# Optimization experiments

Hardware: AMD Instinct MI355X
Metric: run time of the kernel (lower is better)

The kernel has to match this reference:

```python
import jax, jax.numpy as jnp
import numpy as np

# Config matching init_kwargs: layer_nb=1 -> stride 16, image 608x608 -> 38x38 grid
B, CIN, H, W = 32, 512, 38, 38
NA, NC = 3, 80
STRIDE = 16.0
ANCHORS = np.array([[30.0, 61.0], [62.0, 45.0], [59.0, 119.0]], dtype=np.float32)


def setup_inputs() -> dict:
    key = jax.random.key(0)
    k1, k2, k3 = jax.random.split(key, 3)
    xin = jax.random.normal(k1, (B, CIN, H, W), dtype=jnp.float32)
    # 1x1 conv weight stored as (out_ch, in_ch); out_ch = NA*(NC+5) = 255
    conv_w = jax.random.normal(k2, (NA * (NC + 5), CIN), dtype=jnp.float32) * 0.02
    conv_b = jax.random.normal(k3, (NA * (NC + 5),), dtype=jnp.float32) * 0.01
    return {"xin": xin, "conv_w": conv_w, "conv_b": conv_b}


def reference(xin, conv_w, conv_b):
    # 1x1 conv == channel GEMM; fuse the NCHW->NHWC permute into the einsum
    fm = jnp.einsum('bchw,oc->bhwo', xin, conv_w) + conv_b  # [B,H,W,255]
    fm = fm.reshape(B, H, W, NA, NC + 5)
    tx, ty, tw, th = fm[..., 0], fm[..., 1], fm[..., 2], fm[..., 3]
    # grid offsets (precomputed via broadcasting instead of per-call numpy rebuild)
    x_off = jnp.arange(W, dtype=fm.dtype)[None, None, :, None]   # broadcast over B,H,NA
    y_off = jnp.arange(H, dtype=fm.dtype)[None, :, None, None]   # broadcast over B,W,NA
    anchors = jnp.asarray(ANCHORS, dtype=fm.dtype)               # [NA,2]
    bx = (jax.nn.sigmoid(tx) + x_off) * STRIDE
    by = (jax.nn.sigmoid(ty) + y_off) * STRIDE
    bw = jnp.exp(tw) * anchors[:, 0]
    bh = jnp.exp(th) * anchors[:, 1]
    boxes = jnp.stack([bx, by, bw, bh], axis=-1)                 # [B,H,W,NA,4]
    # concat decoded boxes with raw objectness + class logits -> [B,H,W,NA,85]
    return jnp.concatenate([boxes, fm[..., 4:]], axis=-1)
```

## Files before the change

### kernel.cpp

```cpp
#include <hip/hip_runtime.h>
#include <cstdint>
#include <cstddef>

#define CIN_K  512
#define WW_    38
#define BHW    1444
#define NOUT   255
#define MTOT   46208

#define KCH    256
#define ROW_E  260
#define EP_DW  260

typedef __attribute__((ext_vector_type(8))) short  bf16x8;
typedef __attribute__((ext_vector_type(4))) float  floatx4;

static __device__ __forceinline__ unsigned f2bf(float f) {
    unsigned u = __builtin_bit_cast(unsigned, f);
    return (u + 0x7FFFu + ((u >> 16) & 1u)) >> 16;
}

__global__ void conv_w_to_bf16(const float* __restrict__ cw,
                               unsigned short* __restrict__ wb) {
    int tg   = blockIdx.x * 256 + threadIdx.x;
    int base = tg * 8;
    int n    = base >> 9;
    unsigned rr[4] = {0u, 0u, 0u, 0u};
    if (n < NOUT) {
        float4 v0 = *(const float4*)(cw + base);
        float4 v1 = *(const float4*)(cw + base + 4);
        rr[0] = f2bf(v0.x) | (f2bf(v0.y) << 16);
        rr[1] = f2bf(v0.z) | (f2bf(v0.w) << 16);
        rr[2] = f2bf(v1.x) | (f2bf(v1.y) << 16);
        rr[3] = f2bf(v1.z) | (f2bf(v1.w) << 16);
    }
    *(uint4*)(wb + base) = *(uint4*)rr;
}

__global__ __launch_bounds__(256, 4)
void yolo_head(const float* __restrict__ xin,
               const unsigned short* __restrict__ wb,
               const float* __restrict__ cb,
               float* __restrict__ out)
{
    __shared__ unsigned smem[64 * (ROW_E / 2)];
    unsigned short* As = (unsigned short*)smem;

    const int t    = threadIdx.x;
    const int w    = t >> 6;
    const int lane = t & 63;
    const int l15  = lane & 15;
    const int q    = lane >> 4;
    const int m0   = blockIdx.x * 64;

    const int mq4 = (t & 15) * 4;
    const int kq4 = (t >> 4) * 4;
    const int m4  = m0 + mq4;
    const int bi  = m4 / BHW;
    const int hw  = m4 - bi * BHW;
    const float* pb0 = xin + (size_t)bi * (CIN_K * BHW) + hw;

    floatx4 acc[4][4];
#pragma unroll
    for (int i = 0; i < 4; ++i)
#pragma unroll
        for (int j = 0; j < 4; ++j)
            acc[i][j] = (floatx4){0.f, 0.f, 0.f, 0.f};

    const unsigned short* pbw = wb + (size_t)(w * 64 + l15) * CIN_K + q * 8;

#pragma unroll
    for (int ck = 0; ck < 2; ++ck) {
        if (ck) __syncthreads();

#pragma unroll
        for (int it = 0; it < 4; ++it) {
            const int kl = it * 64 + kq4;
            alignas(16) float vv[4][4];
#pragma unroll
            for (int kk = 0; kk < 4; ++kk)
                *(float4*)&vv[kk][0] =
                    *(const float4*)(pb0 + (size_t)(ck * KCH + kl + kk) * BHW);
#pragma unroll
            for (int r = 0; r < 4; ++r) {
                unsigned lo = f2bf(vv[0][r]) | (f2bf(vv[1][r]) << 16);
                unsigned hi = f2bf(vv[2][r]) | (f2bf(vv[3][r]) << 16);
                uint2 pk = make_uint2(lo, hi);
                *(uint2*)(&As[(mq4 + r) * ROW_E + kl]) = pk;
            }
        }
        __syncthreads();

#pragma unroll
        for (int kc = 0; kc < 8; ++kc) {
            bf16x8 bfr[4], af[4];
#pragma unroll
            for (int j = 0; j < 4; ++j) {
                uint4 bv = *(const uint4*)(pbw + (size_t)j * 16 * CIN_K
                                           + ck * KCH + kc * 32);
                bfr[j] = __builtin_bit_cast(bf16x8, bv);
            }
#pragma unroll
            for (int i = 0; i < 4; ++i) {
                int4 av = *(const int4*)(&As[(i * 16 + l15) * ROW_E + kc * 32 + q * 8]);
                af[i] = __builtin_bit_cast(bf16x8, av);
            }
#pragma unroll
            for (int i = 0; i < 4; ++i)
#pragma unroll
                for (int j = 0; j < 4; ++j)
                    acc[i][j] = __builtin_amdgcn_mfma_f32_16x16x32_bf16(
                                    af[i], bfr[j], acc[i][j], 0, 0, 0);
        }
    }

#pragma unroll
    for (int j = 0; j < 4; ++j) {
        int   n    = w * 64 + j * 16 + l15;
        int   nc   = n < NOUT ? n : NOUT - 1;
        int   ai   = nc / 85;
        int   ji   = nc - ai * 85;
        float bias = cb[nc];
        float aw   = (ai == 0) ? 30.f : (ai == 1) ? 62.f : 59.f;
        float ah   = (ai == 0) ? 61.f : (ai == 1) ? 45.f : 119.f;
#pragma unroll
        for (int i = 0; i < 4; ++i)
#pragma unroll
            for (int r = 0; r < 4; ++r) {
                int   md  = m0 + i * 16 + q * 4 + r;
                int   rem = md % BHW;
                int   hh  = rem / WW_;
                float v   = acc[i][j][r] + bias;
                float res;
                if (ji == 0)      res = (1.f / (1.f + __expf(-v)) + (float)(rem - hh * WW_)) * 16.f;
                else if (ji == 1) res = (1.f / (1.f + __expf(-v)) + (float)hh) * 16.f;
                else if (ji == 2) res = __expf(v) * aw;
                else if (ji == 3) res = __expf(v) * ah;
                else              res = v;
                acc[i][j][r] = res;
            }
    }

    float* EP = (float*)smem;
#pragma unroll
    for (int p = 0; p < 2; ++p) {
        __syncthreads();
#pragma unroll
        for (int i2 = 0; i2 < 2; ++i2) {
            const int i = p * 2 + i2;
#pragma unroll
            for (int j = 0; j < 4; ++j)
#pragma unroll
                for (int r = 0; r < 4; ++r)
                    EP[(i2 * 16 + q * 4 + r) * EP_DW + w * 64 + j * 16 + l15] =
                        acc[i][j][r];
        }
        __syncthreads();

        const float* EPb = (const float*)smem + (w * 8) * EP_DW;
        float*       ob  = out + (size_t)(m0 + p * 32 + w * 8) * NOUT;
#pragma unroll
        for (int s2 = 0; s2 < 8; ++s2) {
            int f4 = s2 * 64 + lane;
            if (f4 < 510) {
                int   f = f4 * 4;
                float vs[4];
#pragma unroll
                for (int e = 0; e < 4; ++e) {
                    int fe = f + e;
                    int mr = fe / NOUT;
                    int x  = fe - mr * NOUT;
                    vs[e]  = EPb[mr * EP_DW + x];
                }
                *(float4*)(ob + f) = make_float4(vs[0], vs[1], vs[2], vs[3]);
            }
        }
    }
}

extern "C" void kernel_launch(void* const* d_in, const int* in_sizes, int n_in,
                              void* d_out, int out_size, void* d_ws, size_t ws_size,
                              hipStream_t stream) {
    const float* xin = (const float*)d_in[0];
    const float* cw  = (const float*)d_in[1];
    const float* cb  = (const float*)d_in[2];
    float*       out = (float*)d_out;
    unsigned short* wb = (unsigned short*)d_ws;

    hipLaunchKernelGGL(conv_w_to_bf16, dim3(64), dim3(256), 0, stream, cw, wb);
    hipLaunchKernelGGL(yolo_head, dim3(MTOT / 64), dim3(256), 0, stream,
                       xin, wb, cb, out);
}
```

Measured before the change: 181.3 us.

## Remap workgroups per XCD, use packed bf16 convert, store epilogue directly

Blocks are remapped so each XCD handles a contiguous range of M tiles, which should improve L2 locality across the 722 blocks. The manual f32-to-bf16 rounding is replaced by the packed hardware conversion intrinsic. The LDS-staged, coalesced epilogue is removed and each lane writes its results straight to global memory. That drops two barriers and the LDS traffic, but the scalar stores are strided by 255 floats and coalesce poorly.

```diff
diff --git a/kernel.cpp b/kernel.cpp
--- a/kernel.cpp
+++ b/kernel.cpp
@@ -1,4 +1,5 @@
 #include <hip/hip_runtime.h>
+#include <hip/hip_bf16.h>
 #include <cstdint>
 #include <cstddef>
 
@@ -8,9 +9,9 @@
 #define NOUT   255
 #define MTOT   46208
 
+#define BM     64
 #define KCH    256
 #define ROW_E  260
-#define EP_DW  260
 
 typedef __attribute__((ext_vector_type(8))) short  bf16x8;
 typedef __attribute__((ext_vector_type(4))) float  floatx4;
@@ -18,6 +19,13 @@
 static __device__ __forceinline__ unsigned f2bf(float f) {
     unsigned u = __builtin_bit_cast(unsigned, f);
     return (u + 0x7FFFu + ((u >> 16) & 1u)) >> 16;
+}
+
+static __device__ __forceinline__ unsigned pk2bf(float a, float b) {
+    __hip_bfloat162 h = __float22bfloat162_rn(make_float2(a, b));
+    unsigned r;
+    __builtin_memcpy(&r, &h, 4);
+    return r;
 }
 
 __global__ void conv_w_to_bf16(const float* __restrict__ cw,
@@ -43,7 +51,7 @@
                const float* __restrict__ cb,
                float* __restrict__ out)
 {
-    __shared__ unsigned smem[64 * (ROW_E / 2)];
+    __shared__ unsigned smem[BM * (ROW_E / 2)];
     unsigned short* As = (unsigned short*)smem;
 
     const int t    = threadIdx.x;
@@ -51,7 +59,12 @@
     const int lane = t & 63;
     const int l15  = lane & 15;
     const int q    = lane >> 4;
-    const int m0   = blockIdx.x * 64;
+
+    const int orig = blockIdx.x;
+    const int xcd  = orig & 7;
+    const int rank = orig >> 3;
+    const int wgid = (xcd < 2 ? xcd * 91 : 182 + (xcd - 2) * 90) + rank;
+    const int m0   = wgid * BM;
 
     const int mq4 = (t & 15) * 4;
     const int kq4 = (t >> 4) * 4;
@@ -83,10 +96,9 @@
                     *(const float4*)(pb0 + (size_t)(ck * KCH + kl + kk) * BHW);
 #pragma unroll
             for (int r = 0; r < 4; ++r) {
-                unsigned lo = f2bf(vv[0][r]) | (f2bf(vv[1][r]) << 16);
-                unsigned hi = f2bf(vv[2][r]) | (f2bf(vv[3][r]) << 16);
-                uint2 pk = make_uint2(lo, hi);
-                *(uint2*)(&As[(mq4 + r) * ROW_E + kl]) = pk;
+                unsigned lo = pk2bf(vv[0][r], vv[1][r]);
+                unsigned hi = pk2bf(vv[2][r], vv[3][r]);
+                *(uint2*)(&As[(mq4 + r) * ROW_E + kl]) = make_uint2(lo, hi);
             }
         }
         __syncthreads();
@@ -117,7 +129,8 @@
 #pragma unroll
     for (int j = 0; j < 4; ++j) {
         int   n    = w * 64 + j * 16 + l15;
-        int   nc   = n < NOUT ? n : NOUT - 1;
+        bool  ok   = n < NOUT;
+        int   nc   = ok ? n : NOUT - 1;
         int   ai   = nc / 85;
         int   ji   = nc - ai * 85;
         float bias = cb[nc];
@@ -137,44 +150,8 @@
                 else if (ji == 2) res = __expf(v) * aw;
                 else if (ji == 3) res = __expf(v) * ah;
                 else              res = v;
-                acc[i][j][r] = res;
+                if (ok) out[(size_t)md * NOUT + n] = res;
             }
-    }
-
-    float* EP = (float*)smem;
-#pragma unroll
-    for (int p = 0; p < 2; ++p) {
-        __syncthreads();
-#pragma unroll
-        for (int i2 = 0; i2 < 2; ++i2) {
-            const int i = p * 2 + i2;
-#pragma unroll
-            for (int j = 0; j < 4; ++j)
-#pragma unroll
-                for (int r = 0; r < 4; ++r)
-                    EP[(i2 * 16 + q * 4 + r) * EP_DW + w * 64 + j * 16 + l15] =
-                        acc[i][j][r];
-        }
-        __syncthreads();
-
-        const float* EPb = (const float*)smem + (w * 8) * EP_DW;
-        float*       ob  = out + (size_t)(m0 + p * 32 + w * 8) * NOUT;
-#pragma unroll
-        for (int s2 = 0; s2 < 8; ++s2) {
-            int f4 = s2 * 64 + lane;
-            if (f4 < 510) {
-                int   f = f4 * 4;
-                float vs[4];
-#pragma unroll
-                for (int e = 0; e < 4; ++e) {
-                    int fe = f + e;
-                    int mr = fe / NOUT;
-                    int x  = fe - mr * NOUT;
-                    vs[e]  = EPb[mr * EP_DW + x];
-                }
-                *(float4*)(ob + f) = make_float4(vs[0], vs[1], vs[2], vs[3]);
-            }
-        }
     }
 }
 
@@ -188,6 +165,6 @@
     unsigned short* wb = (unsigned short*)d_ws;
 
     hipLaunchKernelGGL(conv_w_to_bf16, dim3(64), dim3(256), 0, stream, cw, wb);
-    hipLaunchKernelGGL(yolo_head, dim3(MTOT / 64), dim3(256), 0, stream,
+    hipLaunchKernelGGL(yolo_head, dim3(MTOT / BM), dim3(256), 0, stream,
                        xin, wb, cb, out);
 }
```

Result: slower. 192.6 us (+6.2%).
